# Performance work log

Hardware: AMD Instinct MI355X
Metric: run time of the kernel (lower is better)

Reference implementation:

```python
import jax, jax.numpy as jnp
import numpy as np
import math

C = 768          # channels
D = 768          # mod_features
HEADS = 16
CH = C // HEADS  # per-head dim
WIN = (8, 8)     # window size (h, w)
SHIFTED = True
EPS = 1e-5


def setup_inputs() -> dict:
    key = jax.random.key(0)
    ks = jax.random.split(key, 16)
    x = jax.random.normal(ks[0], (8, 64, 64, C), dtype=jnp.float32)
    mod = jax.random.normal(ks[1], (8, D), dtype=jnp.float32)
    s = 0.02
    # AdaLN-zero MLP: Linear(D,D) -> SiLU -> Linear(D, 6C) with weight * 0.01
    ada_w1 = jax.random.normal(ks[2], (D, D), dtype=jnp.float32) * s
    ada_b1 = jnp.zeros((D,), dtype=jnp.float32)
    ada_w2 = jax.random.normal(ks[3], (D, 6 * C), dtype=jnp.float32) * s * 0.01
    ada_b2 = jnp.zeros((6 * C,), dtype=jnp.float32)
    # RoPE theta: amplitude * direction, shape (spatial, C//2)
    amplitude = 10000.0 ** (-jax.random.uniform(ks[4], (2, C // 2)))
    direction = jax.random.normal(ks[5], (2, C // 2))
    direction = direction / jnp.linalg.norm(direction, axis=0, keepdims=True)
    theta = (amplitude * direction).astype(jnp.float32)
    # MSA: qkv + output projection
    qkv_w = jax.random.normal(ks[6], (C, 3 * C), dtype=jnp.float32) * s
    qkv_b = jnp.zeros((3 * C,), dtype=jnp.float32)
    proj_w = jax.random.normal(ks[7], (C, C), dtype=jnp.float32) * s
    proj_b = jnp.zeros((C,), dtype=jnp.float32)
    # MLP: Linear(C,4C) -> SiLU -> Linear(4C,C)
    mlp_w1 = jax.random.normal(ks[8], (C, 4 * C), dtype=jnp.float32) * s
    mlp_b1 = jnp.zeros((4 * C,), dtype=jnp.float32)
    mlp_w2 = jax.random.normal(ks[9], (4 * C, C), dtype=jnp.float32) * s
    mlp_b2 = jnp.zeros((C,), dtype=jnp.float32)
    return dict(x=x, mod=mod, ada_w1=ada_w1, ada_b1=ada_b1, ada_w2=ada_w2,
                ada_b2=ada_b2, theta=theta, qkv_w=qkv_w, qkv_b=qkv_b,
                proj_w=proj_w, proj_b=proj_b, mlp_w1=mlp_w1, mlp_b1=mlp_b1,
                mlp_w2=mlp_w2, mlp_b2=mlp_b2)


def layer_norm(x):
    # parameter-free LayerNorm over last dim (torch.var_mean: unbiased)
    mean = jnp.mean(x, axis=-1, keepdims=True)
    var = jnp.var(x, axis=-1, keepdims=True, ddof=1)
    return (x - mean) * jax.lax.rsqrt(var + EPS)


def apply_rope(q, th):
    # q: (..., H, L, CH), th: (H, L, CH//2); rotate consecutive channel pairs
    qr, qi = q[..., 0::2], q[..., 1::2]
    cos, sin = jnp.cos(th), jnp.sin(th)
    outr = qr * cos - qi * sin
    outi = qr * sin + qi * cos
    return jnp.stack([outr, outi], axis=-1).reshape(q.shape)


def swin_block(x, mod, ada_w1, ada_b1, ada_w2, ada_b2, theta,
               qkv_w, qkv_b, proj_w, proj_b, mlp_w1, mlp_b1, mlp_w2, mlp_b2):
    B, Hd, Wd, _ = x.shape
    wh, ww = WIN
    L = wh * ww
    # AdaLN-zero modulation -> 6 chunks of C, broadcast over spatial dims
    m = jax.nn.silu(mod @ ada_w1 + ada_b1) @ ada_w2 + ada_b2  # (B, 6C)
    a1, b1, c1, a2, b2, c2 = [m[:, i * C:(i + 1) * C][:, None, None, :]
                               for i in range(6)]
    # RoPE angles from window token indices
    ih, iw = jnp.meshgrid(jnp.arange(wh), jnp.arange(ww), indexing='ij')
    idx = jnp.stack([ih.ravel(), iw.ravel()], axis=-1).astype(x.dtype)  # (L, 2)
    th = idx @ theta                                   # (L, C//2)
    th = th.reshape(L, HEADS, CH // 2).transpose(1, 0, 2)  # (HEADS, L, CH//2)
    # pre-attention modulated norm
    y = (a1 + 1.0) * layer_norm(x) + b1
    if SHIFTED:
        y = jnp.roll(y, (wh // 2, ww // 2), axis=(1, 2))
    # group into windows: (B, nH, nW, L, C)
    nH, nW = Hd // wh, Wd // ww
    y = y.reshape(B, nH, wh, nW, ww, C).transpose(0, 1, 3, 2, 4, 5)
    y = y.reshape(B, nH, nW, L, C)
    # windowed multi-head self-attention with RoPE
    qkv = y @ qkv_w + qkv_b
    q, k, v = jnp.split(qkv, 3, axis=-1)

    def heads(t):  # (..., L, C) -> (..., HEADS, L, CH)
        return jnp.swapaxes(t.reshape(B, nH, nW, L, HEADS, CH), -2, -3)

    q, k, v = heads(q), heads(k), heads(v)
    q = apply_rope(q, th)
    k = apply_rope(k, th)
    scale = 1.0 / math.sqrt(CH)
    att = jax.nn.softmax(jnp.einsum('...hlc,...hmc->...hlm', q, k) * scale,
                         axis=-1)
    o = jnp.einsum('...hlm,...hmc->...hlc', att, v)
    o = jnp.swapaxes(o, -2, -3).reshape(B, nH, nW, L, C)
    y = o @ proj_w + proj_b
    # ungroup windows
    y = y.reshape(B, nH, nW, wh, ww, C).transpose(0, 1, 3, 2, 4, 5)
    y = y.reshape(B, Hd, Wd, C)
    if SHIFTED:
        y = jnp.roll(y, (-(wh // 2), -(ww // 2)), axis=(1, 2))
    # gated residual 1 (variance preserving)
    y = (x + c1 * y) * jax.lax.rsqrt(1.0 + c1 * c1)
    # modulated norm + MLP
    z = (a2 + 1.0) * layer_norm(y) + b2
    z = jax.nn.silu(z @ mlp_w1 + mlp_b1) @ mlp_w2 + mlp_b2
    # gated residual 2 (note: uses original x, as in source)
    y = (x + c2 * z) * jax.lax.rsqrt(1.0 + c2 * c2)
    return y


def reference(x, mod, ada_w1, ada_b1, ada_w2, ada_b2, theta, qkv_w, qkv_b,
              proj_w, proj_b, mlp_w1, mlp_b1, mlp_w2, mlp_b2):
    return swin_block(x, mod, ada_w1, ada_b1, ada_w2, ada_b2, theta,
                      qkv_w, qkv_b, proj_w, proj_b, mlp_w1, mlp_b1,
                      mlp_w2, mlp_b2)
```

## Files before the change

kernel.cpp:

```cpp
#include <hip/hip_runtime.h>
#include <stdint.h>
#include <stddef.h>


typedef __bf16 bf16;
typedef __bf16 bf16x8 __attribute__((ext_vector_type(8)));
typedef float  f32x4  __attribute__((ext_vector_type(4)));

__global__ __launch_bounds__(256) void transpose_f32(
    const float* __restrict__ in, bf16* __restrict__ out, int K, int N) {
  __shared__ bf16 tile[32][33];
  const int k0 = blockIdx.x * 32, n0 = blockIdx.y * 32;
  const int tx = threadIdx.x & 31, ty = threadIdx.x >> 5;
#pragma unroll
  for (int j = 0; j < 32; j += 8)
    tile[ty + j][tx] = (bf16)in[(size_t)(k0 + ty + j) * N + n0 + tx];
  __syncthreads();
#pragma unroll
  for (int j = 0; j < 32; j += 8)
    out[(size_t)(n0 + ty + j) * K + k0 + tx] = tile[tx][ty + j];
}

__global__ __launch_bounds__(256) void ada1_kernel(
    const float* __restrict__ mod, const float* __restrict__ w1,
    const float* __restrict__ b1, float* __restrict__ h) {
  const int b = blockIdx.x, o0 = blockIdx.y * 32, t = threadIdx.x;
  const int o = t & 31, kg = t >> 5;
  __shared__ float sm[768];
  for (int j = t; j < 768; j += 256) sm[j] = mod[b * 768 + j];
  __syncthreads();
  float acc = 0.f;
  const int kb = kg * 96;
#pragma unroll 4
  for (int k = 0; k < 96; ++k)
    acc += sm[kb + k] * w1[(size_t)(kb + k) * 768 + o0 + o];
  __shared__ float red[8][32];
  red[kg][o] = acc;
  __syncthreads();
  if (t < 32) {
    float v = red[0][o] + red[1][o] + red[2][o] + red[3][o] + red[4][o] +
              red[5][o] + red[6][o] + red[7][o] + b1[o0 + o];
    h[b * 768 + o0 + o] = v / (1.f + __expf(-v));
  }
}

__global__ __launch_bounds__(256) void ada2_kernel(
    const float* __restrict__ h, const float* __restrict__ w2,
    const float* __restrict__ b2, float* __restrict__ m) {
  const int b = blockIdx.x, o0 = blockIdx.y * 64, t = threadIdx.x;
  const int o = t & 63, kg = t >> 6;
  __shared__ float sh[768];
  for (int j = t; j < 768; j += 256) sh[j] = h[b * 768 + j];
  __syncthreads();
  float acc = 0.f;
  const int kb = kg * 192;
  const float* wp = w2 + (size_t)kb * 4608 + o0 + o;
#pragma unroll 4
  for (int k = 0; k < 192; ++k) acc += sh[kb + k] * wp[(size_t)k * 4608];
  __shared__ float red[4][64];
  red[kg][o] = acc;
  __syncthreads();
  if (t < 64) {
    m[b * 4608 + o0 + o] =
        red[0][o] + red[1][o] + red[2][o] + red[3][o] + b2[o0 + o];
  }
}

template <int SRCF32>
__global__ __launch_bounds__(256) void ln_mod_kernel(
    const void* __restrict__ src, const float* __restrict__ mvec,
    bf16* __restrict__ dst, int shifted) {
  const int t = threadIdx.x;
  const int outTok = blockIdx.x;
  int b, srcTok, aseg, bseg;
  if (shifted) {
    const int win = outTok >> 6, l = outTok & 63;
    b = win >> 6;
    const int wl = win & 63;
    const int hr = ((wl >> 3) << 3) | (l >> 3);
    const int wr = ((wl & 7) << 3) | (l & 7);
    const int hh = (hr + 60) & 63, ww = (wr + 60) & 63;
    srcTok = (b << 12) | (hh << 6) | ww;
    aseg = 0; bseg = 1;
  } else {
    srcTok = outTok; b = outTok >> 12; aseg = 3; bseg = 4;
  }
  float v[3];
#pragma unroll
  for (int j = 0; j < 3; ++j) {
    const size_t idx = (size_t)srcTok * 768 + t + j * 256;
    v[j] = SRCF32 ? ((const float*)src)[idx] : (float)((const bf16*)src)[idx];
  }
  float s = v[0] + v[1] + v[2];
  float q = v[0] * v[0] + v[1] * v[1] + v[2] * v[2];
#pragma unroll
  for (int o = 1; o < 64; o <<= 1) {
    s += __shfl_xor(s, o, 64);
    q += __shfl_xor(q, o, 64);
  }
  __shared__ float rS[4], rQ[4];
  const int wave = t >> 6, lane = t & 63;
  if (lane == 0) { rS[wave] = s; rQ[wave] = q; }
  __syncthreads();
  const float S = rS[0] + rS[1] + rS[2] + rS[3];
  const float Q = rQ[0] + rQ[1] + rQ[2] + rQ[3];
  const float mean = S * (1.f / 768.f);
  const float var = (Q - S * mean) * (1.f / 767.f);
  const float rs = rsqrtf(var + 1e-5f);
  const float* mb = mvec + b * 4608;
#pragma unroll
  for (int j = 0; j < 3; ++j) {
    const int c = t + j * 256;
    const float a = mb[aseg * 768 + c], bb = mb[bseg * 768 + c];
    dst[(size_t)outTok * 768 + c] = (bf16)((a + 1.f) * ((v[j] - mean) * rs) + bb);
  }
}

template <int MODE>
__global__ __launch_bounds__(256) void gemm_bt(
    const bf16* __restrict__ A, const bf16* __restrict__ Bt,
    const float* __restrict__ bias, void* __restrict__ outv, int N, int K,
    int mOff, const float* __restrict__ xres, const float* __restrict__ mvec) {
  __shared__ __align__(16) bf16 sA[128 * 32];
  __shared__ __align__(16) bf16 sB[128 * 32];
  const int t = threadIdx.x;
  const int wave = t >> 6, lane = t & 63;
  const int quad = lane >> 4, l16 = lane & 15;
  const int m0 = blockIdx.x * 128, n0 = blockIdx.y * 128;
  const int wm = (wave & 1) * 64, wn = (wave >> 1) * 64;

  const bf16* gA0 = A + (size_t)(m0 + (t >> 2)) * K + (t & 3) * 8;
  const bf16* gA1 = gA0 + (size_t)64 * K;
  const bf16* gB0 = Bt + (size_t)(n0 + (t >> 2)) * K + (t & 3) * 8;
  const bf16* gB1 = gB0 + (size_t)64 * K;
  bf16* wA0 = sA + t * 8;
  bf16* wA1 = wA0 + 2048;
  bf16* wB0 = sB + t * 8;
  bf16* wB1 = wB0 + 2048;

  f32x4 acc[4][4];
#pragma unroll
  for (int i = 0; i < 4; ++i)
#pragma unroll
    for (int j = 0; j < 4; ++j) acc[i][j] = (f32x4){0.f, 0.f, 0.f, 0.f};

  for (int k0 = 0; k0 < K; k0 += 32) {
    const bf16x8 a0 = *(const bf16x8*)gA0;
    const bf16x8 a1 = *(const bf16x8*)gA1;
    const bf16x8 b0 = *(const bf16x8*)gB0;
    const bf16x8 b1 = *(const bf16x8*)gB1;
    gA0 += 32; gA1 += 32; gB0 += 32; gB1 += 32;
    __syncthreads();
    *(bf16x8*)wA0 = a0;
    *(bf16x8*)wA1 = a1;
    *(bf16x8*)wB0 = b0;
    *(bf16x8*)wB1 = b1;
    __syncthreads();
    bf16x8 aF[4], bF[4];
#pragma unroll
    for (int i = 0; i < 4; ++i)
      aF[i] = *(const bf16x8*)&sA[(wm + i * 16 + l16) * 32 + quad * 8];
#pragma unroll
    for (int i = 0; i < 4; ++i)
      bF[i] = *(const bf16x8*)&sB[(wn + i * 16 + l16) * 32 + quad * 8];
#pragma unroll
    for (int mt = 0; mt < 4; ++mt)
#pragma unroll
      for (int nt = 0; nt < 4; ++nt)
        acc[mt][nt] = __builtin_amdgcn_mfma_f32_16x16x32_bf16(
            aF[mt], bF[nt], acc[mt][nt], 0, 0, 0);
  }

#pragma unroll
  for (int mt = 0; mt < 4; ++mt) {
#pragma unroll
    for (int nt = 0; nt < 4; ++nt) {
      const int col = n0 + wn + nt * 16 + l16;
      const float bv = bias[col];
#pragma unroll
      for (int r = 0; r < 4; ++r) {
        const int row = m0 + wm + mt * 16 + quad * 4 + r;
        const float v = acc[mt][nt][r] + bv;
        if (MODE == 0) {
          ((bf16*)outv)[(size_t)row * N + col] = (bf16)v;
        } else if (MODE == 1) {
          ((bf16*)outv)[(size_t)row * N + col] = (bf16)(v / (1.f + __expf(-v)));
        } else if (MODE == 2) {
          const int grow = row + mOff;
          const int win = grow >> 6, l = grow & 63;
          const int b = win >> 6, wl = win & 63;
          const int hr = ((wl >> 3) << 3) | (l >> 3);
          const int wr = ((wl & 7) << 3) | (l & 7);
          const int hh = (hr + 60) & 63, ww = (wr + 60) & 63;
          const size_t sp = ((size_t)(b << 12)) | (hh << 6) | ww;
          const float c1 = mvec[b * 4608 + 1536 + col];
          const float xv = xres[sp * 768 + col];
          ((bf16*)outv)[sp * 768 + col] =
              (bf16)((xv + c1 * v) * rsqrtf(1.f + c1 * c1));
        } else {
          const int grow = row + mOff;
          const int b = grow >> 12;
          const float c2 = mvec[b * 4608 + 3840 + col];
          const float xv = xres[(size_t)grow * 768 + col];
          ((float*)outv)[(size_t)grow * 768 + col] =
              (xv + c2 * v) * rsqrtf(1.f + c2 * c2);
        }
      }
    }
  }
}

__global__ __launch_bounds__(256) void attn_win(
    const bf16* __restrict__ qkv, const float* __restrict__ theta,
    bf16* __restrict__ ao, int winBase) {
  __shared__ __align__(16) bf16 sQ[64 * 64];
  __shared__ __align__(16) bf16 sK[64 * 64];
  __shared__ __align__(16) bf16 sVT[48 * 64];
  __shared__ __align__(16) bf16 sP[64 * 64];
  const int t = threadIdx.x;
  const int winL = blockIdx.x >> 4, head = blockIdx.x & 15;
  const bf16* qrow = qkv + (size_t)winL * 64 * 2304;

  for (int i = t; i < 3072; i += 256) {
    const int mat = i / 1536;
    const int p = i - mat * 1536;
    const int l = p / 24, d = p - (p / 24) * 24;
    const float ih = (float)(l >> 3), iw = (float)(l & 7);
    const float th = ih * theta[head * 24 + d] + iw * theta[384 + head * 24 + d];
    const float sn = __sinf(th), cs = __cosf(th);
    const size_t base = (size_t)l * 2304 + mat * 768 + head * 48 + 2 * d;
    const float qr = (float)qrow[base];
    const float qi = (float)qrow[base + 1];
    bf16* dst = mat ? sK : sQ;
    dst[l * 64 + 2 * d]     = (bf16)(qr * cs - qi * sn);
    dst[l * 64 + 2 * d + 1] = (bf16)(qr * sn + qi * cs);
  }
  for (int i = t; i < 2048; i += 256) {
    const int mat = i >> 10, r = i & 1023;
    (mat ? sK : sQ)[(r >> 4) * 64 + 48 + (r & 15)] = (bf16)0.f;
  }
  for (int i = t; i < 3072; i += 256) {
    const int l = i / 48, c = i - (i / 48) * 48;
    sVT[c * 64 + l] = qrow[(size_t)l * 2304 + 1536 + head * 48 + c];
  }
  __syncthreads();

  const int wave = t >> 6, lane = t & 63;
  const int quad = lane >> 4, l16 = lane & 15;

  bf16x8 qf0 = *(const bf16x8*)&sQ[(wave * 16 + l16) * 64 + quad * 8];
  bf16x8 qf1 = *(const bf16x8*)&sQ[(wave * 16 + l16) * 64 + 32 + quad * 8];
  f32x4 sc[4];
#pragma unroll
  for (int nt = 0; nt < 4; ++nt) {
    sc[nt] = (f32x4){0.f, 0.f, 0.f, 0.f};
    bf16x8 kf0 = *(const bf16x8*)&sK[(nt * 16 + l16) * 64 + quad * 8];
    bf16x8 kf1 = *(const bf16x8*)&sK[(nt * 16 + l16) * 64 + 32 + quad * 8];
    sc[nt] = __builtin_amdgcn_mfma_f32_16x16x32_bf16(qf0, kf0, sc[nt], 0, 0, 0);
    sc[nt] = __builtin_amdgcn_mfma_f32_16x16x32_bf16(qf1, kf1, sc[nt], 0, 0, 0);
  }

  const float scale = 0.14433756729740643f;
#pragma unroll
  for (int r = 0; r < 4; ++r) {
    float pv[4], mx = -3.4e38f;
#pragma unroll
    for (int nt = 0; nt < 4; ++nt) {
      pv[nt] = sc[nt][r] * scale;
      mx = fmaxf(mx, pv[nt]);
    }
#pragma unroll
    for (int o = 1; o < 16; o <<= 1) mx = fmaxf(mx, __shfl_xor(mx, o, 64));
    float sum = 0.f;
#pragma unroll
    for (int nt = 0; nt < 4; ++nt) {
      pv[nt] = __expf(pv[nt] - mx);
      sum += pv[nt];
    }
#pragma unroll
    for (int o = 1; o < 16; o <<= 1) sum += __shfl_xor(sum, o, 64);
    const float inv = 1.f / sum;
    const int row = wave * 16 + quad * 4 + r;
#pragma unroll
    for (int nt = 0; nt < 4; ++nt)
      sP[row * 64 + nt * 16 + l16] = (bf16)(pv[nt] * inv);
  }
  __syncthreads();

  bf16x8 pf0 = *(const bf16x8*)&sP[(wave * 16 + l16) * 64 + quad * 8];
  bf16x8 pf1 = *(const bf16x8*)&sP[(wave * 16 + l16) * 64 + 32 + quad * 8];
#pragma unroll
  for (int nt = 0; nt < 3; ++nt) {
    f32x4 oc = (f32x4){0.f, 0.f, 0.f, 0.f};
    bf16x8 vf0 = *(const bf16x8*)&sVT[(nt * 16 + l16) * 64 + quad * 8];
    bf16x8 vf1 = *(const bf16x8*)&sVT[(nt * 16 + l16) * 64 + 32 + quad * 8];
    oc = __builtin_amdgcn_mfma_f32_16x16x32_bf16(pf0, vf0, oc, 0, 0, 0);
    oc = __builtin_amdgcn_mfma_f32_16x16x32_bf16(pf1, vf1, oc, 0, 0, 0);
#pragma unroll
    for (int r = 0; r < 4; ++r) {
      const int row = wave * 16 + quad * 4 + r;
      ao[((size_t)(winBase + winL) * 64 + row) * 768 + head * 48 + nt * 16 +
         l16] = (bf16)oc[r];
    }
  }
}

extern "C" void kernel_launch(void* const* d_in, const int* in_sizes, int n_in,
                              void* d_out, int out_size, void* d_ws,
                              size_t ws_size, hipStream_t stream) {
  const float* x      = (const float*)d_in[0];
  const float* mod    = (const float*)d_in[1];
  const float* ada_w1 = (const float*)d_in[2];
  const float* ada_b1 = (const float*)d_in[3];
  const float* ada_w2 = (const float*)d_in[4];
  const float* ada_b2 = (const float*)d_in[5];
  const float* theta  = (const float*)d_in[6];
  const float* qkv_w  = (const float*)d_in[7];
  const float* qkv_b  = (const float*)d_in[8];
  const float* proj_w = (const float*)d_in[9];
  const float* proj_b = (const float*)d_in[10];
  const float* mlp_w1 = (const float*)d_in[11];
  const float* mlp_b1 = (const float*)d_in[12];
  const float* mlp_w2 = (const float*)d_in[13];
  const float* mlp_b2 = (const float*)d_in[14];
  float* outF = (float*)d_out;
  bf16* UP = (bf16*)d_out + 25165824;

  char* ws = (char*)d_ws;
  size_t o = 0;
  auto alloc = [&](size_t bytes) -> char* {
    char* p = ws + o;
    o += (bytes + 255) & ~(size_t)255;
    return p;
  };
  bf16* wT_qkv  = (bf16*)alloc((size_t)2304 * 768 * 2);
  bf16* wT_proj = (bf16*)alloc((size_t)768 * 768 * 2);
  bf16* wT_m1   = (bf16*)alloc((size_t)3072 * 768 * 2);
  bf16* wT_m2   = (bf16*)alloc((size_t)768 * 3072 * 2);
  float* hada   = (float*)alloc((size_t)8 * 768 * 4);
  float* mvec   = (float*)alloc((size_t)8 * 4608 * 4);
  bf16* Y  = (bf16*)alloc((size_t)32768 * 768 * 2);

  const size_t scBig = (size_t)16384 * 3072 * 2;
  const size_t scSml = (size_t)4096 * 3072 * 2;
  const int big = (ws_size >= o + scBig + (4 << 20)) ? 1 : 0;
  bf16* SC = (bf16*)alloc(big ? scBig : scSml);
  const int CHR = big ? 16384 : 4096;
  const int NCH = 32768 / CHR;

  transpose_f32<<<dim3(24, 72), 256, 0, stream>>>(qkv_w, wT_qkv, 768, 2304);
  transpose_f32<<<dim3(24, 24), 256, 0, stream>>>(proj_w, wT_proj, 768, 768);
  transpose_f32<<<dim3(24, 96), 256, 0, stream>>>(mlp_w1, wT_m1, 768, 3072);
  transpose_f32<<<dim3(96, 24), 256, 0, stream>>>(mlp_w2, wT_m2, 3072, 768);
  ada1_kernel<<<dim3(8, 24), 256, 0, stream>>>(mod, ada_w1, ada_b1, hada);
  ada2_kernel<<<dim3(8, 72), 256, 0, stream>>>(hada, ada_w2, ada_b2, mvec);

  ln_mod_kernel<1><<<32768, 256, 0, stream>>>(x, mvec, Y, 1);

  for (int c = 0; c < NCH; ++c) {
    gemm_bt<0><<<dim3(CHR / 128, 18), 256, 0, stream>>>(
        Y + (size_t)c * CHR * 768, wT_qkv, qkv_b, SC, 2304, 768, 0, nullptr,
        mvec);
    attn_win<<<(CHR / 64) * 16, 256, 0, stream>>>(SC, theta, UP,
                                                  c * (CHR / 64));
  }

  gemm_bt<2><<<dim3(256, 6), 256, 0, stream>>>(UP, wT_proj, proj_b, Y, 768,
                                               768, 0, x, mvec);

  ln_mod_kernel<0><<<32768, 256, 0, stream>>>(Y, mvec, UP, 0);

  for (int c = 0; c < NCH; ++c) {
    gemm_bt<1><<<dim3(CHR / 128, 24), 256, 0, stream>>>(
        UP + (size_t)c * CHR * 768, wT_m1, mlp_b1, SC, 3072, 768, 0, nullptr,
        mvec);
    gemm_bt<3><<<dim3(CHR / 128, 6), 256, 0, stream>>>(
        SC, wT_m2, mlp_b2, outF, 768, 3072, c * CHR, x, mvec);
  }
  (void)in_sizes; (void)n_in; (void)out_size;
}
```

Baseline: 1.308 ms.

## Double-buffer GEMM tiles with direct global-to-LDS loads and allow full-size chunk

The bf16 GEMM now loads A/B tiles straight from global memory into LDS with global_load_lds, into two LDS buffers, so the next K-slice is prefetched while MFMAs run on the current one. This replaces the register-staged load and the two barriers per iteration with one barrier. Separately, the host picks a 32768-row chunk when the workspace is large enough, so the qkv/attention stage runs in a single pass. LDS use doubles, which may lower occupancy. The single barrier per step has to correctly order the async LDS writes against the reads of the other buffer.

```diff
diff --git a/kernel.cpp b/kernel.cpp
--- a/kernel.cpp
+++ b/kernel.cpp
@@ -6,6 +6,11 @@
 typedef __bf16 bf16;
 typedef __bf16 bf16x8 __attribute__((ext_vector_type(8)));
 typedef float  f32x4  __attribute__((ext_vector_type(4)));
+
+#define GLDS16(gp, lp)                                              \
+  __builtin_amdgcn_global_load_lds(                                 \
+      (const __attribute__((address_space(1))) void*)(gp),          \
+      (__attribute__((address_space(3))) void*)(lp), 16, 0, 0)
 
 __global__ __launch_bounds__(256) void transpose_f32(
     const float* __restrict__ in, bf16* __restrict__ out, int K, int N) {
@@ -121,8 +126,8 @@
     const bf16* __restrict__ A, const bf16* __restrict__ Bt,
     const float* __restrict__ bias, void* __restrict__ outv, int N, int K,
     int mOff, const float* __restrict__ xres, const float* __restrict__ mvec) {
-  __shared__ __align__(16) bf16 sA[128 * 32];
-  __shared__ __align__(16) bf16 sB[128 * 32];
+  __shared__ __align__(16) bf16 sA[2][128 * 32];
+  __shared__ __align__(16) bf16 sB[2][128 * 32];
   const int t = threadIdx.x;
   const int wave = t >> 6, lane = t & 63;
   const int quad = lane >> 4, l16 = lane & 15;
@@ -133,10 +138,7 @@
   const bf16* gA1 = gA0 + (size_t)64 * K;
   const bf16* gB0 = Bt + (size_t)(n0 + (t >> 2)) * K + (t & 3) * 8;
   const bf16* gB1 = gB0 + (size_t)64 * K;
-  bf16* wA0 = sA + t * 8;
-  bf16* wA1 = wA0 + 2048;
-  bf16* wB0 = sB + t * 8;
-  bf16* wB1 = wB0 + 2048;
+  const int ldsOff = wave * 512;
 
   f32x4 acc[4][4];
 #pragma unroll
@@ -144,31 +146,36 @@
 #pragma unroll
     for (int j = 0; j < 4; ++j) acc[i][j] = (f32x4){0.f, 0.f, 0.f, 0.f};
 
+  GLDS16(gA0, &sA[0][ldsOff]);
+  GLDS16(gA1, &sA[0][ldsOff + 2048]);
+  GLDS16(gB0, &sB[0][ldsOff]);
+  GLDS16(gB1, &sB[0][ldsOff + 2048]);
+  __syncthreads();
+
+  int cur = 0;
   for (int k0 = 0; k0 < K; k0 += 32) {
-    const bf16x8 a0 = *(const bf16x8*)gA0;
-    const bf16x8 a1 = *(const bf16x8*)gA1;
-    const bf16x8 b0 = *(const bf16x8*)gB0;
-    const bf16x8 b1 = *(const bf16x8*)gB1;
-    gA0 += 32; gA1 += 32; gB0 += 32; gB1 += 32;
-    __syncthreads();
-    *(bf16x8*)wA0 = a0;
-    *(bf16x8*)wA1 = a1;
-    *(bf16x8*)wB0 = b0;
-    *(bf16x8*)wB1 = b1;
-    __syncthreads();
+    if (k0 + 32 < K) {
+      const int nxt = cur ^ 1, kk = k0 + 32;
+      GLDS16(gA0 + kk, &sA[nxt][ldsOff]);
+      GLDS16(gA1 + kk, &sA[nxt][ldsOff + 2048]);
+      GLDS16(gB0 + kk, &sB[nxt][ldsOff]);
+      GLDS16(gB1 + kk, &sB[nxt][ldsOff + 2048]);
+    }
     bf16x8 aF[4], bF[4];
 #pragma unroll
     for (int i = 0; i < 4; ++i)
-      aF[i] = *(const bf16x8*)&sA[(wm + i * 16 + l16) * 32 + quad * 8];
+      aF[i] = *(const bf16x8*)&sA[cur][(wm + i * 16 + l16) * 32 + quad * 8];
 #pragma unroll
     for (int i = 0; i < 4; ++i)
-      bF[i] = *(const bf16x8*)&sB[(wn + i * 16 + l16) * 32 + quad * 8];
+      bF[i] = *(const bf16x8*)&sB[cur][(wn + i * 16 + l16) * 32 + quad * 8];
 #pragma unroll
     for (int mt = 0; mt < 4; ++mt)
 #pragma unroll
       for (int nt = 0; nt < 4; ++nt)
         acc[mt][nt] = __builtin_amdgcn_mfma_f32_16x16x32_bf16(
             aF[mt], bF[nt], acc[mt][nt], 0, 0, 0);
+    __syncthreads();
+    cur ^= 1;
   }
 
 #pragma unroll
@@ -341,11 +348,10 @@
   float* mvec   = (float*)alloc((size_t)8 * 4608 * 4);
   bf16* Y  = (bf16*)alloc((size_t)32768 * 768 * 2);
 
-  const size_t scBig = (size_t)16384 * 3072 * 2;
-  const size_t scSml = (size_t)4096 * 3072 * 2;
-  const int big = (ws_size >= o + scBig + (4 << 20)) ? 1 : 0;
-  bf16* SC = (bf16*)alloc(big ? scBig : scSml);
-  const int CHR = big ? 16384 : 4096;
+  int CHR = 4096;
+  if (ws_size >= o + (size_t)32768 * 3072 * 2 + (4 << 20)) CHR = 32768;
+  else if (ws_size >= o + (size_t)16384 * 3072 * 2 + (4 << 20)) CHR = 16384;
+  bf16* SC = (bf16*)alloc((size_t)CHR * 3072 * 2);
   const int NCH = 32768 / CHR;
 
   transpose_f32<<<dim3(24, 72), 256, 0, stream>>>(qkv_w, wT_qkv, 768, 2304);
```

After: 1.257 ms. 3.9% less time.
